# Kernel tuning notes

Hardware: AMD Instinct MI355X
Metric: run time of the kernel (lower is better)

The kernel has to match this reference:

```python
import jax, jax.numpy as jnp
import numpy as np

D_MODEL = 1024
EXPAND = 2
D_INNER = EXPAND * D_MODEL          # 2048
HEADDIM = 64
NHEADS = D_INNER // HEADDIM         # 32
D_STATE = 128
NGROUPS = 1
D_CONV = 4
CONV_DIM = D_INNER + 2 * NGROUPS * D_STATE   # 2304
D_IN_PROJ = 2 * D_INNER + 2 * NGROUPS * D_STATE + NHEADS  # 4384
EPS = 1e-5


def setup_inputs() -> dict:
    key = jax.random.key(0)
    ks = jax.random.split(key, 12)
    x = jax.random.normal(ks[0], (2, 2048, D_MODEL), dtype=jnp.float32)
    in_proj_w = jax.random.normal(ks[1], (D_IN_PROJ, D_MODEL), dtype=jnp.float32) * 0.02
    conv_w = jax.random.normal(ks[2], (CONV_DIM, D_CONV), dtype=jnp.float32) * 0.2
    conv_b = jax.random.normal(ks[3], (CONV_DIM,), dtype=jnp.float32) * 0.02
    # dt_bias from inverse-softplus of dt ~ U(1e-3, 0.1)
    dt = jnp.exp(jax.random.uniform(ks[4], (NHEADS,)) * (np.log(0.1) - np.log(1e-3)) + np.log(1e-3))
    dt_bias = dt + jnp.log(-jnp.expm1(-dt))
    A_log = jnp.log(jax.random.uniform(ks[5], (NHEADS,), minval=1.0, maxval=16.0))
    D_skip = jnp.ones((NHEADS,), dtype=jnp.float32)
    norm_w = jnp.ones((D_INNER,), dtype=jnp.float32)
    out_w = jax.random.normal(ks[6], (D_MODEL, D_INNER), dtype=jnp.float32) * 0.02
    ln_g = jnp.ones((D_MODEL,), dtype=jnp.float32)
    ln_b = jnp.zeros((D_MODEL,), dtype=jnp.float32)
    return {"x": x, "in_proj_w": in_proj_w, "conv_w": conv_w, "conv_b": conv_b,
            "dt_bias": dt_bias, "A_log": A_log, "D_skip": D_skip, "norm_w": norm_w,
            "out_w": out_w, "ln_g": ln_g, "ln_b": ln_b}


def _depthwise_causal_conv(x, w, b):
    # x: (B, L, C); w: (C, K); causal depthwise conv (torch Conv1d groups=C, padding=K-1, truncated)
    K = w.shape[1]
    y = jax.lax.conv_general_dilated(
        x.transpose(0, 2, 1), w[:, None, :], (1,), [(K - 1, 0)],
        feature_group_count=w.shape[0], dimension_numbers=("NCH", "OIH", "NCH"))
    return y.transpose(0, 2, 1) + b


def _ssd_scan(xh, dt, A, Bm, Cm):
    # xh: (B,L,H,P), dt: (B,L,H), A: (H,), Bm/Cm: (B,L,N)  (ngroups=1)
    dA = jnp.exp(dt * A)  # (B,L,H)

    def step(h, inp):
        dA_t, dt_t, x_t, B_t, C_t = inp
        h = dA_t[..., None, None] * h + jnp.einsum("bh,bhp,bn->bhpn", dt_t, x_t, B_t)
        y = jnp.einsum("bhpn,bn->bhp", h, C_t)
        return h, y

    Bsz, L, H, P = xh.shape
    N = Bm.shape[-1]
    h0 = jnp.zeros((Bsz, H, P, N), dtype=xh.dtype)
    inputs = (dA.transpose(1, 0, 2), dt.transpose(1, 0, 2),
              xh.transpose(1, 0, 2, 3), Bm.transpose(1, 0, 2), Cm.transpose(1, 0, 2))
    _, ys = jax.lax.scan(step, h0, inputs)  # ys: (L,B,H,P)
    return ys.transpose(1, 0, 2, 3)


def reference(x, in_proj_w, conv_w, conv_b, dt_bias, A_log, D_skip, norm_w, out_w, ln_g, ln_b):
    B, L, D = x.shape
    residual = x  # D is a multiple of 8 -> pad branch is a no-op

    zxbcdt = jnp.einsum("bld,ed->ble", x, in_proj_w)  # (B,L,D_IN_PROJ)
    z = zxbcdt[..., :D_INNER]
    xBC = zxbcdt[..., D_INNER:D_INNER + CONV_DIM]
    dt = jax.nn.softplus(zxbcdt[..., D_INNER + CONV_DIM:] + dt_bias)  # (B,L,H)

    xBC = jax.nn.silu(_depthwise_causal_conv(xBC, conv_w, conv_b))
    xh = xBC[..., :D_INNER].reshape(B, L, NHEADS, HEADDIM)
    Bm = xBC[..., D_INNER:D_INNER + D_STATE]
    Cm = xBC[..., D_INNER + D_STATE:]

    A = -jnp.exp(A_log)  # (H,)
    y = _ssd_scan(xh, dt, A, Bm, Cm)          # (B,L,H,P)
    y = y + xh * D_skip[None, None, :, None]  # D skip connection
    y = y.reshape(B, L, D_INNER)

    # gated RMSNorm: normalize y * silu(z)
    y = y * jax.nn.silu(z)
    y = y * jax.lax.rsqrt(jnp.mean(y * y, axis=-1, keepdims=True) + EPS) * norm_w

    out = jnp.einsum("ble,de->bld", y, out_w)  # (B,L,D)

    # block LayerNorm + residual (dropout p=0 -> identity)
    mu = jnp.mean(out, axis=-1, keepdims=True)
    var = jnp.mean(jnp.square(out - mu), axis=-1, keepdims=True)
    out = (out - mu) * jax.lax.rsqrt(var + EPS) * ln_g + ln_b
    return out + residual
```

## Files before the change

### kernel.cpp

```cpp
#include <hip/hip_runtime.h>
#include <math.h>

#define D_MODEL   1024
#define D_INNER   2048
#define HEADDIM   64
#define NHEADS    32
#define D_STATE   128
#define D_CONV    4
#define CONV_DIM  2304
#define D_IN_PROJ 4384
#define NPAD      4480
#define LSEQ      2048
#define BATCH     2
#define NROWS     4096
#define NC        32

typedef __attribute__((ext_vector_type(8))) short short8_t;
typedef __attribute__((ext_vector_type(4))) float f32x4;

#define MFMA16(a, b, c) __builtin_amdgcn_mfma_f32_16x16x32_bf16(a, b, c, 0, 0, 0)

#define GLDS(g, l) __builtin_amdgcn_global_load_lds( \
    (const __attribute__((address_space(1))) unsigned int*)(g), \
    (__attribute__((address_space(3))) unsigned int*)(l), 16, 0, 0)

__device__ __forceinline__ unsigned short f2bf(float f) {
  union { float f; unsigned int u; } v; v.f = f;
  unsigned int u = v.u + 0x7FFFu + ((v.u >> 16) & 1u);
  return (unsigned short)(u >> 16);
}
__device__ __forceinline__ float bf2f(unsigned short h) {
  union { unsigned int u; float f; } v; v.u = ((unsigned int)h) << 16;
  return v.f;
}

__device__ __forceinline__ short8_t lds_frag(const unsigned short* base, int row,
                                             int col, int rowlen) {
  int off = (row * rowlen + col) * 2;
  off ^= (row & 7) << 4;
  return *reinterpret_cast<const short8_t*>(
      reinterpret_cast<const char*>(base) + off);
}
__device__ __forceinline__ void lds_w32(unsigned short* base, int row, int col,
                                        int rowlen, unsigned int val) {
  int off = (row * rowlen + col) * 2;
  off ^= (row & 7) << 4;
  *reinterpret_cast<unsigned int*>(reinterpret_cast<char*>(base) + off) = val;
}
__device__ __forceinline__ void lds_w16(unsigned short* base, int row, int col,
                                        int rowlen, unsigned short val) {
  int off = (row * rowlen + col) * 2;
  off ^= (row & 7) << 4;
  *reinterpret_cast<unsigned short*>(reinterpret_cast<char*>(base) + off) = val;
}
__device__ __forceinline__ unsigned short lds_r16(const unsigned short* base,
                                                  int row, int col, int rowlen) {
  int off = (row * rowlen + col) * 2;
  off ^= (row & 7) << 4;
  return *reinterpret_cast<const unsigned short*>(
      reinterpret_cast<const char*>(base) + off);
}

template <int MODE>
__global__ __launch_bounds__(256) void gemm_bf16(
    const unsigned short* __restrict__ A, const unsigned short* __restrict__ B,
    void* __restrict__ Cout, float* __restrict__ dtraw, int N, int K) {
  __shared__ unsigned short sA[128 * 64];
  __shared__ unsigned short sB[128 * 64];
  const int tid = threadIdx.x;
  const int lin = blockIdx.y * gridDim.x + blockIdx.x;
  const int cpx = (gridDim.x * gridDim.y) >> 3;
  const int swz = (lin & 7) * cpx + (lin >> 3);
  const int row0 = (swz / gridDim.x) * 128;
  const int col0 = (swz % gridDim.x) * 128;

  const int l  = tid & 63;
  const int la = l & 15;
  const int lk = (l >> 4) * 8;
  const int w  = tid >> 6;
  const int wr = (w >> 1) * 64;
  const int wc = (w & 1) * 64;

  f32x4 acc[4][4];
  #pragma unroll
  for (int i = 0; i < 4; ++i)
    #pragma unroll
    for (int j = 0; j < 4; ++j) acc[i][j] = (f32x4){0.f, 0.f, 0.f, 0.f};

  for (int k0 = 0; k0 < K; k0 += 64) {
    __syncthreads();
    #pragma unroll
    for (int i = 0; i < 4; ++i) {
      int s = i * 256 + tid;
      int r = s >> 3;
      int j = s & 7;
      int jc = j ^ (r & 7);
      GLDS(&A[(size_t)(row0 + r) * K + k0 + jc * 8], &sA[s * 8]);
      GLDS(&B[(size_t)(col0 + r) * K + k0 + jc * 8], &sB[s * 8]);
    }
    __syncthreads();

    #pragma unroll
    for (int kk = 0; kk < 2; ++kk) {
      short8_t af[4], bfr[4];
      #pragma unroll
      for (int mi = 0; mi < 4; ++mi)
        af[mi] = lds_frag(sA, wr + mi * 16 + la, kk * 32 + lk, 64);
      #pragma unroll
      for (int ni = 0; ni < 4; ++ni)
        bfr[ni] = lds_frag(sB, wc + ni * 16 + la, kk * 32 + lk, 64);
      #pragma unroll
      for (int mi = 0; mi < 4; ++mi)
        #pragma unroll
        for (int ni = 0; ni < 4; ++ni)
          acc[mi][ni] = MFMA16(af[mi], bfr[ni], acc[mi][ni]);
    }
  }

  #pragma unroll
  for (int mi = 0; mi < 4; ++mi)
    #pragma unroll
    for (int ni = 0; ni < 4; ++ni)
      #pragma unroll
      for (int r = 0; r < 4; ++r) {
        int gm = row0 + wr + mi * 16 + (l >> 4) * 4 + r;
        int gn = col0 + wc + ni * 16 + la;
        if (gn < N) {
          if constexpr (MODE == 0) {
            ((float*)Cout)[(size_t)gm * N + gn] = acc[mi][ni][r];
          } else {
            ((unsigned short*)Cout)[(size_t)gm * N + gn] = f2bf(acc[mi][ni][r]);
            if (gn >= N - 32) dtraw[(size_t)gm * 32 + (gn - (N - 32))] = acc[mi][ni][r];
          }
        }
      }
}

__global__ __launch_bounds__(256) void cvt_bf16_kernel(
    const float* __restrict__ src, unsigned short* __restrict__ dst) {
  long i = (long)blockIdx.x * 256 + threadIdx.x;
  float4 a = *reinterpret_cast<const float4*>(&src[i * 8]);
  float4 b = *reinterpret_cast<const float4*>(&src[i * 8 + 4]);
  short8_t o;
  o[0] = (short)f2bf(a.x); o[1] = (short)f2bf(a.y);
  o[2] = (short)f2bf(a.z); o[3] = (short)f2bf(a.w);
  o[4] = (short)f2bf(b.x); o[5] = (short)f2bf(b.y);
  o[6] = (short)f2bf(b.z); o[7] = (short)f2bf(b.w);
  *reinterpret_cast<short8_t*>(&dst[i * 8]) = o;
}

__global__ __launch_bounds__(256) void cvt_w_kernel(
    const float* __restrict__ w, unsigned short* __restrict__ wbf) {
  long i = (long)blockIdx.x * 256 + threadIdx.x;
  int row = (int)(i >> 7);
  int c8  = (int)(i & 127) << 3;
  short8_t o = {0, 0, 0, 0, 0, 0, 0, 0};
  if (row < D_IN_PROJ) {
    float4 a = *reinterpret_cast<const float4*>(&w[(size_t)row * D_MODEL + c8]);
    float4 b = *reinterpret_cast<const float4*>(&w[(size_t)row * D_MODEL + c8 + 4]);
    o[0] = (short)f2bf(a.x); o[1] = (short)f2bf(a.y);
    o[2] = (short)f2bf(a.z); o[3] = (short)f2bf(a.w);
    o[4] = (short)f2bf(b.x); o[5] = (short)f2bf(b.y);
    o[6] = (short)f2bf(b.z); o[7] = (short)f2bf(b.w);
  }
  *reinterpret_cast<short8_t*>(&wbf[(size_t)row * D_MODEL + c8]) = o;
}

__global__ __launch_bounds__(256) void conv_silu_kernel(
    const unsigned short* __restrict__ zxb, const float* __restrict__ conv_w,
    const float* __restrict__ conv_b, unsigned short* __restrict__ xconv) {
  const int c  = blockIdx.x * 256 + threadIdx.x;
  const int l0 = blockIdx.y * 128;
  const int b  = blockIdx.z;
  const unsigned short* src = zxb + ((size_t)b * LSEQ) * D_IN_PROJ + D_INNER + c;
  const float w0 = conv_w[c * 4 + 0], w1 = conv_w[c * 4 + 1];
  const float w2 = conv_w[c * 4 + 2], w3 = conv_w[c * 4 + 3];
  const float bia = conv_b[c];
  float x0 = (l0 >= 3) ? bf2f(src[(size_t)(l0 - 3) * D_IN_PROJ]) : 0.f;
  float x1 = (l0 >= 2) ? bf2f(src[(size_t)(l0 - 2) * D_IN_PROJ]) : 0.f;
  float x2 = (l0 >= 1) ? bf2f(src[(size_t)(l0 - 1) * D_IN_PROJ]) : 0.f;
  unsigned short* dst = xconv + ((size_t)(b * LSEQ + l0)) * CONV_DIM + c;
  #pragma unroll 4
  for (int i = 0; i < 128; ++i) {
    float x3 = bf2f(src[(size_t)(l0 + i) * D_IN_PROJ]);
    float acc = fmaf(w3, x3, fmaf(w2, x2, fmaf(w1, x1, fmaf(w0, x0, bia))));
    float s = acc / (1.f + expf(-acc));
    dst[(size_t)i * CONV_DIM] = f2bf(s);
    x0 = x1; x1 = x2; x2 = x3;
  }
}

__global__ __launch_bounds__(256) void dt_kernel(
    const float* __restrict__ dtraw, const float* __restrict__ dt_bias,
    float* __restrict__ dt_out) {
  int idx = blockIdx.x * 256 + threadIdx.x;
  int h = idx & 31;
  float x = dtraw[idx] + dt_bias[h];
  float dt = (x > 20.f) ? x : log1pf(expf(x));
  dt_out[idx] = dt;
}

__global__ __launch_bounds__(256) void cumsum_kernel(
    const float* __restrict__ dt_s, const float* __restrict__ A_log,
    float* __restrict__ cumL) {
  int u = blockIdx.x * 4 + (threadIdx.x >> 6);
  int lane = threadIdx.x & 63;
  int h = u & 31;
  int bc = u >> 5;
  int row = bc * 64 + lane;
  float A = -expf(A_log[h]);
  float a = dt_s[(size_t)row * NHEADS + h] * A;
  #pragma unroll
  for (int off = 1; off < 64; off <<= 1) {
    float v = __shfl_up(a, off);
    if (lane >= off) a += v;
  }
  cumL[(size_t)u * 64 + lane] = a;
}

__global__ __launch_bounds__(256) void chunkstate_kernel(
    const unsigned short* __restrict__ xconv, const float* __restrict__ dt_s,
    const float* __restrict__ cumL, unsigned short* __restrict__ S) {
  const int bi = blockIdx.x;
  const int h  = bi & 31;
  const int bc = bi >> 5;
  const int row0 = bc * 64;
  const int tid = threadIdx.x;

  __shared__ unsigned short sBT[128 * 64];
  __shared__ unsigned short sXT[64 * 64];
  __shared__ float sw[64];

  if (tid < 64) {
    float L   = cumL[(size_t)bi * 64 + tid];
    float L63 = cumL[(size_t)bi * 64 + 63];
    sw[tid] = dt_s[(size_t)(row0 + tid) * NHEADS + h] * expf(L63 - L);
  }
  __syncthreads();

  #pragma unroll
  for (int i = 0; i < 16; ++i) {
    int idx = tid + i * 256;
    int s = idx >> 6, n2 = idx & 63;
    unsigned int v = *reinterpret_cast<const unsigned int*>(
        &xconv[(size_t)(row0 + s) * CONV_DIM + D_INNER + n2 * 2]);
    lds_w16(sBT, n2 * 2 + 0, s, 64, (unsigned short)v);
    lds_w16(sBT, n2 * 2 + 1, s, 64, (unsigned short)(v >> 16));
  }
  #pragma unroll
  for (int i = 0; i < 16; ++i) {
    int idx = tid + i * 256;
    int s = idx >> 6, p = idx & 63;
    float xv = bf2f(xconv[(size_t)(row0 + s) * CONV_DIM + h * HEADDIM + p]);
    lds_w16(sXT, p, s, 64, f2bf(xv * sw[s]));
  }
  __syncthreads();

  const int w  = tid >> 6;
  const int l  = tid & 63;
  const int la = l & 15;
  const int lk = (l >> 4) * 8;

  f32x4 acc[8];
  #pragma unroll
  for (int i = 0; i < 8; ++i) acc[i] = (f32x4){0.f, 0.f, 0.f, 0.f};

  #pragma unroll
  for (int ks = 0; ks < 2; ++ks) {
    short8_t a = lds_frag(sXT, 16 * w + la, ks * 32 + lk, 64);
    #pragma unroll
    for (int ni = 0; ni < 8; ++ni) {
      short8_t b = lds_frag(sBT, ni * 16 + la, ks * 32 + lk, 64);
      acc[ni] = MFMA16(a, b, acc[ni]);
    }
  }

  unsigned short* dst = S + (size_t)bi * (HEADDIM * D_STATE);
  #pragma unroll
  for (int ni = 0; ni < 8; ++ni)
    #pragma unroll
    for (int r = 0; r < 4; ++r) {
      int p = 16 * w + (l >> 4) * 4 + r;
      int n = ni * 16 + la;
      dst[p * D_STATE + n] = f2bf(acc[ni][r]);
    }
}

__global__ __launch_bounds__(256) void hscan_kernel(
    unsigned short* __restrict__ S, const float* __restrict__ cumL) {
  const int g  = blockIdx.x;
  const int bh = g >> 5;
  const int b  = bh >> 5;
  const int h  = bh & 31;
  const int e  = (g & 31) * 256 + threadIdx.x;

  float H = 0.f;
  #pragma unroll 4
  for (int c = 0; c < NC; ++c) {
    size_t u = (size_t)((b * NC + c) * NHEADS + h);
    float dA = expf(cumL[u * 64 + 63]);
    unsigned short sv = S[u * (HEADDIM * D_STATE) + e];
    S[u * (HEADDIM * D_STATE) + e] = f2bf(H);
    H = dA * H + bf2f(sv);
  }
}

__global__ __launch_bounds__(256) void chunk_kernel(
    const unsigned short* __restrict__ xconv, const float* __restrict__ dt_s,
    const float* __restrict__ cumL, const unsigned short* __restrict__ Hprev,
    const float* __restrict__ D_skip, unsigned short* __restrict__ y) {
  const int bi = blockIdx.x;
  const int h  = bi & 31;
  const int bc = bi >> 5;
  const int row0 = bc * 64;
  const int tid = threadIdx.x;

  __shared__ unsigned short sC[64 * 128];
  __shared__ unsigned short sB[64 * 128];
  __shared__ unsigned short sXT[64 * 64];
  __shared__ unsigned short sP[64 * 64];
  __shared__ float sL[64], sdt[64], seL[64];

  if (tid < 64) {
    float L = cumL[(size_t)bi * 64 + tid];
    sL[tid]  = L;
    seL[tid] = expf(L);
    sdt[tid] = dt_s[(size_t)(row0 + tid) * NHEADS + h];
  }

  #pragma unroll
  for (int i = 0; i < 8; ++i) {
    int idx = tid + i * 256;
    int r = idx >> 5, q = idx & 31;
    short8_t v = *reinterpret_cast<const short8_t*>(
        &xconv[(size_t)(row0 + r) * CONV_DIM + D_INNER + q * 8]);
    unsigned int u0 = (unsigned int)(unsigned short)v[0] |
                      ((unsigned int)(unsigned short)v[1] << 16);
    unsigned int u1 = (unsigned int)(unsigned short)v[2] |
                      ((unsigned int)(unsigned short)v[3] << 16);
    unsigned int u2 = (unsigned int)(unsigned short)v[4] |
                      ((unsigned int)(unsigned short)v[5] << 16);
    unsigned int u3 = (unsigned int)(unsigned short)v[6] |
                      ((unsigned int)(unsigned short)v[7] << 16);
    unsigned short* dstb = (q < 16) ? sB : sC;
    int cq = (q & 15) * 8;
    lds_w32(dstb, r, cq + 0, 128, u0);
    lds_w32(dstb, r, cq + 2, 128, u1);
    lds_w32(dstb, r, cq + 4, 128, u2);
    lds_w32(dstb, r, cq + 6, 128, u3);
  }
  #pragma unroll
  for (int i = 0; i < 16; ++i) {
    int idx = tid + i * 256;
    int s = idx >> 6, p = idx & 63;
    lds_w16(sXT, p, s, 64,
            xconv[(size_t)(row0 + s) * CONV_DIM + h * HEADDIM + p]);
  }
  __syncthreads();

  const int w  = tid >> 6;
  const int l  = tid & 63;
  const int la = l & 15;
  const int lk = (l >> 4) * 8;
  const int t0 = 16 * w;

  f32x4 g[4];
  #pragma unroll
  for (int i = 0; i < 4; ++i) g[i] = (f32x4){0.f, 0.f, 0.f, 0.f};
  #pragma unroll
  for (int ks = 0; ks < 4; ++ks) {
    short8_t a = lds_frag(sC, t0 + la, ks * 32 + lk, 128);
    #pragma unroll
    for (int si = 0; si < 4; ++si) {
      short8_t b = lds_frag(sB, si * 16 + la, ks * 32 + lk, 128);
      g[si] = MFMA16(a, b, g[si]);
    }
  }
  #pragma unroll
  for (int si = 0; si < 4; ++si)
    #pragma unroll
    for (int r = 0; r < 4; ++r) {
      int t = t0 + (l >> 4) * 4 + r;
      int s = si * 16 + la;
      float m = 0.f;
      if (s <= t) m = expf(sL[t] - sL[s]) * sdt[s] * g[si][r];
      lds_w16(sP, t, s, 64, f2bf(m));
    }
  __syncthreads();

  f32x4 o[4];
  #pragma unroll
  for (int i = 0; i < 4; ++i) o[i] = (f32x4){0.f, 0.f, 0.f, 0.f};

  const unsigned short* hb = Hprev + (size_t)bi * (HEADDIM * D_STATE);
  #pragma unroll
  for (int ks = 0; ks < 4; ++ks) {
    short8_t a = lds_frag(sC, t0 + la, ks * 32 + lk, 128);
    #pragma unroll
    for (int si = 0; si < 4; ++si) {
      int p = si * 16 + la;
      short8_t b = *reinterpret_cast<const short8_t*>(
          &hb[p * D_STATE + ks * 32 + lk]);
      o[si] = MFMA16(a, b, o[si]);
    }
  }
  #pragma unroll
  for (int si = 0; si < 4; ++si)
    #pragma unroll
    for (int r = 0; r < 4; ++r) {
      int t = t0 + (l >> 4) * 4 + r;
      o[si][r] *= seL[t];
    }
  #pragma unroll
  for (int ks = 0; ks < 2; ++ks) {
    short8_t a = lds_frag(sP, t0 + la, ks * 32 + lk, 64);
    #pragma unroll
    for (int si = 0; si < 4; ++si) {
      short8_t b = lds_frag(sXT, si * 16 + la, ks * 32 + lk, 64);
      o[si] = MFMA16(a, b, o[si]);
    }
  }
  const float Dh = D_skip[h];
  #pragma unroll
  for (int si = 0; si < 4; ++si)
    #pragma unroll
    for (int r = 0; r < 4; ++r) {
      int t = t0 + (l >> 4) * 4 + r;
      int p = si * 16 + la;
      float xv = bf2f(lds_r16(sXT, p, t, 64));
      y[(size_t)(row0 + t) * D_INNER + h * HEADDIM + p] = f2bf(o[si][r] + Dh * xv);
    }
}

__global__ __launch_bounds__(256) void gate_rms_kernel(
    unsigned short* __restrict__ y, const unsigned short* __restrict__ zxb,
    const float* __restrict__ norm_w) {
  const int row = blockIdx.x;
  const int tid = threadIdx.x;
  short8_t zv = *reinterpret_cast<const short8_t*>(
      &zxb[(size_t)row * D_IN_PROJ + tid * 8]);
  short8_t yv = *reinterpret_cast<short8_t*>(
      &y[(size_t)row * D_INNER + tid * 8]);
  float v[8];
  float acc = 0.f;
  #pragma unroll
  for (int i = 0; i < 8; ++i) {
    float z  = bf2f((unsigned short)zv[i]);
    float ys = bf2f((unsigned short)yv[i]);
    float gz = z / (1.f + expf(-z));
    float val = ys * gz;
    v[i] = val;
    acc = fmaf(val, val, acc);
  }
  #pragma unroll
  for (int off = 32; off; off >>= 1) acc += __shfl_xor(acc, off);
  __shared__ float wsum[4];
  if ((tid & 63) == 0) wsum[tid >> 6] = acc;
  __syncthreads();
  float total = wsum[0] + wsum[1] + wsum[2] + wsum[3];
  float scale = rsqrtf(total / (float)D_INNER + 1e-5f);
  short8_t o;
  #pragma unroll
  for (int i = 0; i < 8; ++i)
    o[i] = (short)f2bf(v[i] * scale * norm_w[tid * 8 + i]);
  *reinterpret_cast<short8_t*>(&y[(size_t)row * D_INNER + tid * 8]) = o;
}

__global__ __launch_bounds__(256) void ln_kernel(
    const float* __restrict__ o, const float* __restrict__ x,
    const float* __restrict__ lng, const float* __restrict__ lnb,
    float* __restrict__ out) {
  const int row = blockIdx.x;
  const int tid = threadIdx.x;
  float v[4];
  float s = 0.f, s2 = 0.f;
  #pragma unroll
  for (int i = 0; i < 4; ++i) {
    int d = i * 256 + tid;
    float t = o[(size_t)row * D_MODEL + d];
    v[i] = t;
    s += t;
    s2 = fmaf(t, t, s2);
  }
  #pragma unroll
  for (int off = 32; off; off >>= 1) {
    s  += __shfl_xor(s, off);
    s2 += __shfl_xor(s2, off);
  }
  __shared__ float sa[4], sb[4];
  if ((tid & 63) == 0) { sa[tid >> 6] = s; sb[tid >> 6] = s2; }
  __syncthreads();
  s  = sa[0] + sa[1] + sa[2] + sa[3];
  s2 = sb[0] + sb[1] + sb[2] + sb[3];
  float mu  = s / (float)D_MODEL;
  float var = s2 / (float)D_MODEL - mu * mu;
  float inv = rsqrtf(var + 1e-5f);
  #pragma unroll
  for (int i = 0; i < 4; ++i) {
    int d = i * 256 + tid;
    out[(size_t)row * D_MODEL + d] =
        (v[i] - mu) * inv * lng[d] + lnb[d] + x[(size_t)row * D_MODEL + d];
  }
}

extern "C" void kernel_launch(void* const* d_in, const int* in_sizes, int n_in,
                              void* d_out, int out_size, void* d_ws, size_t ws_size,
                              hipStream_t stream) {
  const float* x         = (const float*)d_in[0];
  const float* in_proj_w = (const float*)d_in[1];
  const float* conv_w    = (const float*)d_in[2];
  const float* conv_b    = (const float*)d_in[3];
  const float* dt_bias   = (const float*)d_in[4];
  const float* A_log     = (const float*)d_in[5];
  const float* D_skip    = (const float*)d_in[6];
  const float* norm_w    = (const float*)d_in[7];
  const float* out_w     = (const float*)d_in[8];
  const float* ln_g      = (const float*)d_in[9];
  const float* ln_b      = (const float*)d_in[10];
  float* out = (float*)d_out;

  char* ws = (char*)d_ws;
  unsigned short* zxb   = (unsigned short*)ws;
  float* outpre         = (float*)ws;
  char* p = ws + (size_t)NROWS * D_IN_PROJ * 2;
  float* dtraw = (float*)p;            p += (size_t)NROWS * 32 * 4;
  float* dt_s  = (float*)p;            p += (size_t)NROWS * 32 * 4;
  float* cumL  = (float*)p;            p += (size_t)BATCH * NC * NHEADS * 64 * 4;
  unsigned short* xconv = (unsigned short*)p;  p += (size_t)NROWS * CONV_DIM * 2;
  unsigned short* schp  = (unsigned short*)p;  p += (size_t)BATCH * NC * NHEADS * HEADDIM * D_STATE * 2;
  unsigned short* ybuf  = (unsigned short*)p;  p += (size_t)NROWS * D_INNER * 2;
  unsigned short* xbf   = (unsigned short*)p;  p += (size_t)NROWS * D_MODEL * 2;
  unsigned short* wbf   = (unsigned short*)p;  p += (size_t)NPAD * D_MODEL * 2;
  unsigned short* owbf  = (unsigned short*)p;

  cvt_bf16_kernel<<<dim3(NROWS * D_MODEL / 8 / 256), dim3(256), 0, stream>>>(
      x, xbf);
  cvt_w_kernel<<<dim3(NPAD * 128 / 256), dim3(256), 0, stream>>>(
      in_proj_w, wbf);
  cvt_bf16_kernel<<<dim3(D_MODEL * D_INNER / 8 / 256), dim3(256), 0, stream>>>(
      out_w, owbf);

  gemm_bf16<1><<<dim3(NPAD / 128, NROWS / 128), dim3(256), 0, stream>>>(
      xbf, wbf, zxb, dtraw, D_IN_PROJ, D_MODEL);

  conv_silu_kernel<<<dim3(CONV_DIM / 256, LSEQ / 128, BATCH), dim3(256), 0, stream>>>(
      zxb, conv_w, conv_b, xconv);

  dt_kernel<<<dim3(NROWS * NHEADS / 256), dim3(256), 0, stream>>>(
      dtraw, dt_bias, dt_s);

  cumsum_kernel<<<dim3(BATCH * NC * NHEADS / 4), dim3(256), 0, stream>>>(
      dt_s, A_log, cumL);

  chunkstate_kernel<<<dim3(BATCH * NC * NHEADS), dim3(256), 0, stream>>>(
      xconv, dt_s, cumL, schp);

  hscan_kernel<<<dim3(BATCH * NHEADS * 32), dim3(256), 0, stream>>>(
      schp, cumL);

  chunk_kernel<<<dim3(BATCH * NC * NHEADS), dim3(256), 0, stream>>>(
      xconv, dt_s, cumL, schp, D_skip, ybuf);

  gate_rms_kernel<<<dim3(NROWS), dim3(256), 0, stream>>>(
      ybuf, zxb, norm_w);

  gemm_bf16<0><<<dim3(D_MODEL / 128, NROWS / 128), dim3(256), 0, stream>>>(
      ybuf, owbf, outpre, nullptr, D_MODEL, D_INNER);

  ln_kernel<<<dim3(NROWS), dim3(256), 0, stream>>>(
      outpre, x, ln_g, ln_b, out);
}
```

Before: 322.3 us.

## Add double-buffered 128x256 in-projection GEMM and fuse dt softplus into cumsum

Replaces the in-projection GEMM with a new 512-thread kernel that computes 128x256 tiles. It double-buffers LDS through async global-to-LDS loads spread across the MFMA sub-steps and raises wave priority during the MFMA blocks. This is meant to overlap memory traffic with compute and reuse each A tile across more columns. The padded weight width grows so the column count divides by 256, which adds some wasted compute on padding. Separately, the softplus dt computation moves into the cumsum kernel, which removes one launch and one round trip of dt through memory.

```diff
diff --git a/kernel.cpp b/kernel.cpp
--- a/kernel.cpp
+++ b/kernel.cpp
@@ -9,7 +9,7 @@
 #define D_CONV    4
 #define CONV_DIM  2304
 #define D_IN_PROJ 4384
-#define NPAD      4480
+#define NPAD      4608
 #define LSEQ      2048
 #define BATCH     2
 #define NROWS     4096
@@ -61,10 +61,115 @@
       reinterpret_cast<const char*>(base) + off);
 }
 
-template <int MODE>
+__global__ __launch_bounds__(512, 1) void gemm8_in(
+    const unsigned short* __restrict__ A, const unsigned short* __restrict__ B,
+    unsigned short* __restrict__ Cout, float* __restrict__ dtraw, int N, int K) {
+  extern __shared__ unsigned short lds8[];
+  const int tid = threadIdx.x;
+  const int gx = gridDim.x;
+  const int lin = blockIdx.y * gx + blockIdx.x;
+  const int cpx = (gx * gridDim.y) >> 3;
+  const int swz = (lin & 7) * cpx + (lin >> 3);
+  const int row0 = (swz / gx) * 128;
+  const int col0 = (swz % gx) * 256;
+
+  const int l  = tid & 63;
+  const int la = l & 15;
+  const int lk = (l >> 4) * 8;
+  const int w  = tid >> 6;
+  const int wm = w >> 2;
+  const int wn = w & 3;
+
+  const int s0 = tid, s1 = tid + 512;
+  const int r0 = s0 >> 3, j0 = ((s0 & 7) ^ (r0 & 7)) * 8;
+  const int r1 = s1 >> 3, j1 = ((s1 & 7) ^ (r1 & 7)) * 8;
+
+  f32x4 acc[4][4];
+  #pragma unroll
+  for (int i = 0; i < 4; ++i)
+    #pragma unroll
+    for (int j = 0; j < 4; ++j) acc[i][j] = (f32x4){0.f, 0.f, 0.f, 0.f};
+
+  const int NT = K >> 6;
+
+  {
+    unsigned short* dA = lds8;
+    unsigned short* dB = lds8 + 8192;
+    GLDS(&A[(size_t)(row0 + r0) * K + j0], &dA[s0 * 8]);
+    GLDS(&A[(size_t)(row0 + r1) * K + j1], &dA[s1 * 8]);
+    GLDS(&B[(size_t)(col0 + r0) * K + j0], &dB[s0 * 8]);
+    GLDS(&B[(size_t)(col0 + r1) * K + j1], &dB[s1 * 8]);
+    GLDS(&B[(size_t)(col0 + 128 + r0) * K + j0], &dB[8192 + s0 * 8]);
+    GLDS(&B[(size_t)(col0 + 128 + r1) * K + j1], &dB[8192 + s1 * 8]);
+  }
+  asm volatile("s_waitcnt vmcnt(0)" ::: "memory");
+  __builtin_amdgcn_s_barrier();
+
+  for (int t = 0; t < NT; ++t) {
+    const int cur = t & 1;
+    const int k1 = (t + 1) << 6;
+    const bool st = (t + 1 < NT);
+    const unsigned short* aB = lds8 + cur * 24576;
+    const unsigned short* bB = lds8 + cur * 24576 + 8192;
+    unsigned short* dA = lds8 + (cur ^ 1) * 24576;
+    unsigned short* dB = dA + 8192;
+
+    #pragma unroll
+    for (int q = 0; q < 4; ++q) {
+      short8_t af[2], bfm[4][2];
+      #pragma unroll
+      for (int kk = 0; kk < 2; ++kk)
+        af[kk] = lds_frag(aB, wm * 64 + q * 16 + la, kk * 32 + lk, 64);
+      #pragma unroll
+      for (int ni = 0; ni < 4; ++ni)
+        #pragma unroll
+        for (int kk = 0; kk < 2; ++kk)
+          bfm[ni][kk] = lds_frag(bB, wn * 64 + ni * 16 + la, kk * 32 + lk, 64);
+      if (q == 0 && st) {
+        GLDS(&A[(size_t)(row0 + r0) * K + k1 + j0], &dA[s0 * 8]);
+        GLDS(&A[(size_t)(row0 + r1) * K + k1 + j1], &dA[s1 * 8]);
+      }
+      if (q == 1 && st) {
+        GLDS(&B[(size_t)(col0 + r0) * K + k1 + j0], &dB[s0 * 8]);
+        GLDS(&B[(size_t)(col0 + r1) * K + k1 + j1], &dB[s1 * 8]);
+      }
+      if (q == 2 && st) {
+        GLDS(&B[(size_t)(col0 + 128 + r0) * K + k1 + j0], &dB[8192 + s0 * 8]);
+        GLDS(&B[(size_t)(col0 + 128 + r1) * K + k1 + j1], &dB[8192 + s1 * 8]);
+      }
+      __builtin_amdgcn_s_barrier();
+      __builtin_amdgcn_s_setprio(1);
+      #pragma unroll
+      for (int ni = 0; ni < 4; ++ni)
+        #pragma unroll
+        for (int kk = 0; kk < 2; ++kk)
+          acc[q][ni] = MFMA16(af[kk], bfm[ni][kk], acc[q][ni]);
+      __builtin_amdgcn_s_setprio(0);
+      if (q == 3) asm volatile("s_waitcnt vmcnt(0)" ::: "memory");
+      __builtin_amdgcn_s_barrier();
+    }
+  }
+
+  #pragma unroll
+  for (int ni = 0; ni < 4; ++ni) {
+    int gn = col0 + wn * 64 + ni * 16 + la;
+    if (gn < N) {
+      #pragma unroll
+      for (int mi = 0; mi < 4; ++mi)
+        #pragma unroll
+        for (int r = 0; r < 4; ++r) {
+          int gm = row0 + wm * 64 + mi * 16 + (l >> 4) * 4 + r;
+          Cout[(size_t)gm * N + gn] = f2bf(acc[mi][ni][r]);
+          if (gn >= N - 32)
+            dtraw[(size_t)gm * 32 + (gn - (N - 32))] = acc[mi][ni][r];
+        }
+    }
+  }
+}
+
 __global__ __launch_bounds__(256) void gemm_bf16(
     const unsigned short* __restrict__ A, const unsigned short* __restrict__ B,
-    void* __restrict__ Cout, float* __restrict__ dtraw, int N, int K) {
+    float* __restrict__ C, int N, int K) {
   __shared__ unsigned short sA[128 * 64];
   __shared__ unsigned short sB[128 * 64];
   const int tid = threadIdx.x;
@@ -125,14 +230,7 @@
       for (int r = 0; r < 4; ++r) {
         int gm = row0 + wr + mi * 16 + (l >> 4) * 4 + r;
         int gn = col0 + wc + ni * 16 + la;
-        if (gn < N) {
-          if constexpr (MODE == 0) {
-            ((float*)Cout)[(size_t)gm * N + gn] = acc[mi][ni][r];
-          } else {
-            ((unsigned short*)Cout)[(size_t)gm * N + gn] = f2bf(acc[mi][ni][r]);
-            if (gn >= N - 32) dtraw[(size_t)gm * 32 + (gn - (N - 32))] = acc[mi][ni][r];
-          }
-        }
+        C[(size_t)gm * N + gn] = acc[mi][ni][r];
       }
 }
 
@@ -190,26 +288,20 @@
   }
 }
 
-__global__ __launch_bounds__(256) void dt_kernel(
+__global__ __launch_bounds__(256) void cumsum_kernel(
     const float* __restrict__ dtraw, const float* __restrict__ dt_bias,
-    float* __restrict__ dt_out) {
-  int idx = blockIdx.x * 256 + threadIdx.x;
-  int h = idx & 31;
-  float x = dtraw[idx] + dt_bias[h];
-  float dt = (x > 20.f) ? x : log1pf(expf(x));
-  dt_out[idx] = dt;
-}
-
-__global__ __launch_bounds__(256) void cumsum_kernel(
-    const float* __restrict__ dt_s, const float* __restrict__ A_log,
+    const float* __restrict__ A_log, float* __restrict__ dt_s,
     float* __restrict__ cumL) {
   int u = blockIdx.x * 4 + (threadIdx.x >> 6);
   int lane = threadIdx.x & 63;
   int h = u & 31;
   int bc = u >> 5;
   int row = bc * 64 + lane;
+  float xr = dtraw[(size_t)row * 32 + h] + dt_bias[h];
+  float dt = (xr > 20.f) ? xr : log1pf(expf(xr));
+  dt_s[(size_t)row * NHEADS + h] = dt;
   float A = -expf(A_log[h]);
-  float a = dt_s[(size_t)row * NHEADS + h] * A;
+  float a = dt * A;
   #pragma unroll
   for (int off = 1; off < 64; off <<= 1) {
     float v = __shfl_up(a, off);
@@ -533,6 +625,9 @@
   unsigned short* wbf   = (unsigned short*)p;  p += (size_t)NPAD * D_MODEL * 2;
   unsigned short* owbf  = (unsigned short*)p;
 
+  (void)hipFuncSetAttribute(reinterpret_cast<const void*>(&gemm8_in),
+                            hipFuncAttributeMaxDynamicSharedMemorySize, 98304);
+
   cvt_bf16_kernel<<<dim3(NROWS * D_MODEL / 8 / 256), dim3(256), 0, stream>>>(
       x, xbf);
   cvt_w_kernel<<<dim3(NPAD * 128 / 256), dim3(256), 0, stream>>>(
@@ -540,17 +635,14 @@
   cvt_bf16_kernel<<<dim3(D_MODEL * D_INNER / 8 / 256), dim3(256), 0, stream>>>(
       out_w, owbf);
 
-  gemm_bf16<1><<<dim3(NPAD / 128, NROWS / 128), dim3(256), 0, stream>>>(
+  gemm8_in<<<dim3(NPAD / 256, NROWS / 128), dim3(512), 98304, stream>>>(
       xbf, wbf, zxb, dtraw, D_IN_PROJ, D_MODEL);
 
   conv_silu_kernel<<<dim3(CONV_DIM / 256, LSEQ / 128, BATCH), dim3(256), 0, stream>>>(
       zxb, conv_w, conv_b, xconv);
 
-  dt_kernel<<<dim3(NROWS * NHEADS / 256), dim3(256), 0, stream>>>(
-      dtraw, dt_bias, dt_s);
-
   cumsum_kernel<<<dim3(BATCH * NC * NHEADS / 4), dim3(256), 0, stream>>>(
-      dt_s, A_log, cumL);
+      dtraw, dt_bias, A_log, dt_s, cumL);
 
   chunkstate_kernel<<<dim3(BATCH * NC * NHEADS), dim3(256), 0, stream>>>(
       xconv, dt_s, cumL, schp);
@@ -564,8 +656,8 @@
   gate_rms_kernel<<<dim3(NROWS), dim3(256), 0, stream>>>(
       ybuf, zxb, norm_w);
 
-  gemm_bf16<0><<<dim3(D_MODEL / 128, NROWS / 128), dim3(256), 0, stream>>>(
-      ybuf, owbf, outpre, nullptr, D_MODEL, D_INNER);
+  gemm_bf16<<<dim3(D_MODEL / 128, NROWS / 128), dim3(256), 0, stream>>>(
+      ybuf, owbf, outpre, D_MODEL, D_INNER);
 
   ln_kernel<<<dim3(NROWS), dim3(256), 0, stream>>>(
       outpre, x, ln_g, ln_b, out);
```

Result: no change. 328.1 us (+1.8%).

## Double-buffer GEMM LDS tiles and fuse conversion and dt kernels

Applied to the files above, without the earlier changes.

Both GEMMs now use two LDS buffers in 64 KB of dynamic shared memory. The next K tile is prefetched with global_load_lds while MFMAs run on the current tile, leaving one barrier per iteration instead of two. The three fp32-to-bf16 conversion kernels become one launch, and the softplus dt computation moves into the cumsum kernel, cutting launch count and one intermediate round trip. Doubling the LDS use may lower occupancy per CU.

```diff
diff --git a/kernel.cpp b/kernel.cpp
--- a/kernel.cpp
+++ b/kernel.cpp
@@ -61,12 +61,23 @@
       reinterpret_cast<const char*>(base) + off);
 }
 
+#define STAGE_TILE(bufA, bufB, kk0)                                        \
+  do {                                                                     \
+    _Pragma("unroll")                                                      \
+    for (int i_ = 0; i_ < 4; ++i_) {                                       \
+      int s_ = i_ * 256 + tid;                                             \
+      int r_ = s_ >> 3;                                                    \
+      int jc_ = ((s_ & 7) ^ (r_ & 7)) * 8;                                 \
+      GLDS(&A[(size_t)(row0 + r_) * K + (kk0) + jc_], &(bufA)[s_ * 8]);    \
+      GLDS(&B[(size_t)(col0 + r_) * K + (kk0) + jc_], &(bufB)[s_ * 8]);    \
+    }                                                                      \
+  } while (0)
+
 template <int MODE>
-__global__ __launch_bounds__(256) void gemm_bf16(
+__global__ __launch_bounds__(256) void gemm_db(
     const unsigned short* __restrict__ A, const unsigned short* __restrict__ B,
     void* __restrict__ Cout, float* __restrict__ dtraw, int N, int K) {
-  __shared__ unsigned short sA[128 * 64];
-  __shared__ unsigned short sB[128 * 64];
+  extern __shared__ unsigned short lds[];
   const int tid = threadIdx.x;
   const int lin = blockIdx.y * gridDim.x + blockIdx.x;
   const int cpx = (gridDim.x * gridDim.y) >> 3;
@@ -87,34 +98,42 @@
     #pragma unroll
     for (int j = 0; j < 4; ++j) acc[i][j] = (f32x4){0.f, 0.f, 0.f, 0.f};
 
-  for (int k0 = 0; k0 < K; k0 += 64) {
-    __syncthreads();
-    #pragma unroll
-    for (int i = 0; i < 4; ++i) {
-      int s = i * 256 + tid;
-      int r = s >> 3;
-      int j = s & 7;
-      int jc = j ^ (r & 7);
-      GLDS(&A[(size_t)(row0 + r) * K + k0 + jc * 8], &sA[s * 8]);
-      GLDS(&B[(size_t)(col0 + r) * K + k0 + jc * 8], &sB[s * 8]);
-    }
-    __syncthreads();
-
+  const int NT = K >> 6;
+
+  {
+    unsigned short* dA = lds;
+    unsigned short* dB = lds + 8192;
+    STAGE_TILE(dA, dB, 0);
+  }
+  asm volatile("s_waitcnt vmcnt(0)" ::: "memory");
+  __builtin_amdgcn_s_barrier();
+
+  for (int t = 0; t < NT; ++t) {
+    const int cur = t & 1;
+    if (t + 1 < NT) {
+      unsigned short* dA = lds + (cur ^ 1) * 16384;
+      unsigned short* dB = dA + 8192;
+      STAGE_TILE(dA, dB, (t + 1) << 6);
+    }
+    const unsigned short* aB = lds + cur * 16384;
+    const unsigned short* bB = aB + 8192;
     #pragma unroll
     for (int kk = 0; kk < 2; ++kk) {
       short8_t af[4], bfr[4];
       #pragma unroll
       for (int mi = 0; mi < 4; ++mi)
-        af[mi] = lds_frag(sA, wr + mi * 16 + la, kk * 32 + lk, 64);
+        af[mi] = lds_frag(aB, wr + mi * 16 + la, kk * 32 + lk, 64);
       #pragma unroll
       for (int ni = 0; ni < 4; ++ni)
-        bfr[ni] = lds_frag(sB, wc + ni * 16 + la, kk * 32 + lk, 64);
+        bfr[ni] = lds_frag(bB, wc + ni * 16 + la, kk * 32 + lk, 64);
       #pragma unroll
       for (int mi = 0; mi < 4; ++mi)
         #pragma unroll
         for (int ni = 0; ni < 4; ++ni)
           acc[mi][ni] = MFMA16(af[mi], bfr[ni], acc[mi][ni]);
     }
+    asm volatile("s_waitcnt vmcnt(0)" ::: "memory");
+    __builtin_amdgcn_s_barrier();
   }
 
   #pragma unroll
@@ -130,40 +149,44 @@
             ((float*)Cout)[(size_t)gm * N + gn] = acc[mi][ni][r];
           } else {
             ((unsigned short*)Cout)[(size_t)gm * N + gn] = f2bf(acc[mi][ni][r]);
-            if (gn >= N - 32) dtraw[(size_t)gm * 32 + (gn - (N - 32))] = acc[mi][ni][r];
+            if (gn >= N - 32)
+              dtraw[(size_t)gm * 32 + (gn - (N - 32))] = acc[mi][ni][r];
           }
         }
       }
 }
 
-__global__ __launch_bounds__(256) void cvt_bf16_kernel(
-    const float* __restrict__ src, unsigned short* __restrict__ dst) {
-  long i = (long)blockIdx.x * 256 + threadIdx.x;
-  float4 a = *reinterpret_cast<const float4*>(&src[i * 8]);
-  float4 b = *reinterpret_cast<const float4*>(&src[i * 8 + 4]);
+__device__ __forceinline__ short8_t cvt8(const float* s) {
+  float4 a = *reinterpret_cast<const float4*>(s);
+  float4 b = *reinterpret_cast<const float4*>(s + 4);
   short8_t o;
   o[0] = (short)f2bf(a.x); o[1] = (short)f2bf(a.y);
   o[2] = (short)f2bf(a.z); o[3] = (short)f2bf(a.w);
   o[4] = (short)f2bf(b.x); o[5] = (short)f2bf(b.y);
   o[6] = (short)f2bf(b.z); o[7] = (short)f2bf(b.w);
-  *reinterpret_cast<short8_t*>(&dst[i * 8]) = o;
-}
-
-__global__ __launch_bounds__(256) void cvt_w_kernel(
-    const float* __restrict__ w, unsigned short* __restrict__ wbf) {
+  return o;
+}
+
+__global__ __launch_bounds__(256) void cvt_all_kernel(
+    const float* __restrict__ x, const float* __restrict__ w,
+    const float* __restrict__ ow, unsigned short* __restrict__ xbf,
+    unsigned short* __restrict__ wbf, unsigned short* __restrict__ owbf) {
+  const long n1 = (long)NROWS * D_MODEL / 8;
+  const long n2 = (long)NPAD * D_MODEL / 8;
   long i = (long)blockIdx.x * 256 + threadIdx.x;
-  int row = (int)(i >> 7);
-  int c8  = (int)(i & 127) << 3;
-  short8_t o = {0, 0, 0, 0, 0, 0, 0, 0};
-  if (row < D_IN_PROJ) {
-    float4 a = *reinterpret_cast<const float4*>(&w[(size_t)row * D_MODEL + c8]);
-    float4 b = *reinterpret_cast<const float4*>(&w[(size_t)row * D_MODEL + c8 + 4]);
-    o[0] = (short)f2bf(a.x); o[1] = (short)f2bf(a.y);
-    o[2] = (short)f2bf(a.z); o[3] = (short)f2bf(a.w);
-    o[4] = (short)f2bf(b.x); o[5] = (short)f2bf(b.y);
-    o[6] = (short)f2bf(b.z); o[7] = (short)f2bf(b.w);
-  }
-  *reinterpret_cast<short8_t*>(&wbf[(size_t)row * D_MODEL + c8]) = o;
+  if (i < n1) {
+    *reinterpret_cast<short8_t*>(&xbf[i * 8]) = cvt8(&x[i * 8]);
+  } else if (i < n1 + n2) {
+    long j = i - n1;
+    int row = (int)(j >> 7);
+    int c8  = (int)(j & 127) << 3;
+    short8_t o = {0, 0, 0, 0, 0, 0, 0, 0};
+    if (row < D_IN_PROJ) o = cvt8(&w[(size_t)row * D_MODEL + c8]);
+    *reinterpret_cast<short8_t*>(&wbf[(size_t)row * D_MODEL + c8]) = o;
+  } else {
+    long j = i - n1 - n2;
+    *reinterpret_cast<short8_t*>(&owbf[j * 8]) = cvt8(&ow[j * 8]);
+  }
 }
 
 __global__ __launch_bounds__(256) void conv_silu_kernel(
@@ -190,26 +213,20 @@
   }
 }
 
-__global__ __launch_bounds__(256) void dt_kernel(
+__global__ __launch_bounds__(256) void cumsum_kernel(
     const float* __restrict__ dtraw, const float* __restrict__ dt_bias,
-    float* __restrict__ dt_out) {
-  int idx = blockIdx.x * 256 + threadIdx.x;
-  int h = idx & 31;
-  float x = dtraw[idx] + dt_bias[h];
-  float dt = (x > 20.f) ? x : log1pf(expf(x));
-  dt_out[idx] = dt;
-}
-
-__global__ __launch_bounds__(256) void cumsum_kernel(
-    const float* __restrict__ dt_s, const float* __restrict__ A_log,
+    const float* __restrict__ A_log, float* __restrict__ dt_s,
     float* __restrict__ cumL) {
   int u = blockIdx.x * 4 + (threadIdx.x >> 6);
   int lane = threadIdx.x & 63;
   int h = u & 31;
   int bc = u >> 5;
   int row = bc * 64 + lane;
+  float xr = dtraw[(size_t)row * 32 + h] + dt_bias[h];
+  float dt = (xr > 20.f) ? xr : log1pf(expf(xr));
+  dt_s[(size_t)row * NHEADS + h] = dt;
   float A = -expf(A_log[h]);
-  float a = dt_s[(size_t)row * NHEADS + h] * A;
+  float a = dt * A;
   #pragma unroll
   for (int off = 1; off < 64; off <<= 1) {
     float v = __shfl_up(a, off);
@@ -533,24 +550,28 @@
   unsigned short* wbf   = (unsigned short*)p;  p += (size_t)NPAD * D_MODEL * 2;
   unsigned short* owbf  = (unsigned short*)p;
 
-  cvt_bf16_kernel<<<dim3(NROWS * D_MODEL / 8 / 256), dim3(256), 0, stream>>>(
-      x, xbf);
-  cvt_w_kernel<<<dim3(NPAD * 128 / 256), dim3(256), 0, stream>>>(
-      in_proj_w, wbf);
-  cvt_bf16_kernel<<<dim3(D_MODEL * D_INNER / 8 / 256), dim3(256), 0, stream>>>(
-      out_w, owbf);
-
-  gemm_bf16<1><<<dim3(NPAD / 128, NROWS / 128), dim3(256), 0, stream>>>(
+  (void)hipFuncSetAttribute(reinterpret_cast<const void*>(&gemm_db<1>),
+                            hipFuncAttributeMaxDynamicSharedMemorySize, 65536);
+  (void)hipFuncSetAttribute(reinterpret_cast<const void*>(&gemm_db<0>),
+                            hipFuncAttributeMaxDynamicSharedMemorySize, 65536);
+
+  {
+    const long n1 = (long)NROWS * D_MODEL / 8;
+    const long n2 = (long)NPAD * D_MODEL / 8;
+    const long n3 = (long)D_MODEL * D_INNER / 8;
+    int nblk = (int)((n1 + n2 + n3) / 256);
+    cvt_all_kernel<<<dim3(nblk), dim3(256), 0, stream>>>(
+        x, in_proj_w, out_w, xbf, wbf, owbf);
+  }
+
+  gemm_db<1><<<dim3(NPAD / 128, NROWS / 128), dim3(256), 65536, stream>>>(
       xbf, wbf, zxb, dtraw, D_IN_PROJ, D_MODEL);
 
   conv_silu_kernel<<<dim3(CONV_DIM / 256, LSEQ / 128, BATCH), dim3(256), 0, stream>>>(
       zxb, conv_w, conv_b, xconv);
 
-  dt_kernel<<<dim3(NROWS * NHEADS / 256), dim3(256), 0, stream>>>(
-      dtraw, dt_bias, dt_s);
-
   cumsum_kernel<<<dim3(BATCH * NC * NHEADS / 4), dim3(256), 0, stream>>>(
-      dt_s, A_log, cumL);
+      dtraw, dt_bias, A_log, dt_s, cumL);
 
   chunkstate_kernel<<<dim3(BATCH * NC * NHEADS), dim3(256), 0, stream>>>(
       xconv, dt_s, cumL, schp);
@@ -564,7 +585,7 @@
   gate_rms_kernel<<<dim3(NROWS), dim3(256), 0, stream>>>(
       ybuf, zxb, norm_w);
 
-  gemm_bf16<0><<<dim3(D_MODEL / 128, NROWS / 128), dim3(256), 0, stream>>>(
+  gemm_db<0><<<dim3(D_MODEL / 128, NROWS / 128), dim3(256), 65536, stream>>>(
       ybuf, owbf, outpre, nullptr, D_MODEL, D_INNER);
 
   ln_kernel<<<dim3(NROWS), dim3(256), 0, stream>>>(
```

Result: faster. 298.8 us (-7.3%).
